# Kernel optimization log

Hardware: AMD Instinct MI355X
Metric: run time of the kernel (lower is better)

Reference implementation:

```python
import jax, jax.numpy as jnp
import numpy as np

N_NODES = 100000
N_EDGES = 1600000
D_IN = 128
D_HID = 64
D_EMB = 64
EDGE_DIM = 2 * D_EMB  # 128
N_CASES = 4
BATCH = 16384
BN_EPS = 1e-5


def gcn_conv(x, src, dst, n, W, b):
    # PyG GCNConv: linear transform, add self-loops, sym-normalized aggregation
    h = x @ W  # [N, out]
    loop = jnp.arange(n, dtype=src.dtype)
    s = jnp.concatenate([src, loop])
    d = jnp.concatenate([dst, loop])
    deg = jax.ops.segment_sum(jnp.ones(s.shape[0], dtype=h.dtype), d, num_segments=n)
    dinv = jnp.where(deg > 0, deg ** -0.5, 0.0)
    norm = dinv[s] * dinv[d]  # [E+N]
    msg = h[s] * norm[:, None]
    return jax.ops.segment_sum(msg, d, num_segments=n) + b


def batchnorm(h, gamma, beta):
    # BatchNorm1d in training mode: biased batch statistics over nodes
    mu = h.mean(0)
    var = jnp.mean((h - mu) ** 2, axis=0)
    return (h - mu) * jax.lax.rsqrt(var + BN_EPS) * gamma + beta


def gcn_net(x, src, dst, n, W1, b1, g, be, W2, b2):
    h = gcn_conv(x, src, dst, n, W1, b1)
    h = jax.nn.relu(batchnorm(h, g, be))
    return gcn_conv(h, src, dst, n, W2, b2)


def setup_inputs() -> dict:
    key = jax.random.key(0)
    ks = jax.random.split(key, 20)
    inp = {
        "x": jax.random.normal(ks[0], (N_NODES, D_IN), dtype=jnp.float32),
        "edge_index": jax.random.randint(ks[1], (2, N_EDGES), 0, N_NODES, dtype=jnp.int32),
        "users_tensor": jax.random.randint(ks[2], (BATCH,), 0, 50000, dtype=jnp.int64) if jax.config.jax_enable_x64 else jax.random.randint(ks[2], (BATCH,), 0, 50000, dtype=jnp.int32),
        "items_tensor": jax.random.randint(ks[3], (BATCH,), 0, N_NODES, dtype=jnp.int32),
    }
    s = 0.05
    # generalized GCN params
    inp["W1g"] = jax.random.normal(ks[4], (D_IN, D_HID), dtype=jnp.float32) * s
    inp["b1g"] = jnp.zeros((D_HID,), jnp.float32)
    inp["g1g"] = jnp.ones((D_HID,), jnp.float32)
    inp["be1g"] = jnp.zeros((D_HID,), jnp.float32)
    inp["W2g"] = jax.random.normal(ks[5], (D_HID, D_EMB), dtype=jnp.float32) * s
    inp["b2g"] = jnp.zeros((D_EMB,), jnp.float32)
    # specific GCN params
    inp["W1s"] = jax.random.normal(ks[6], (D_IN, D_HID), dtype=jnp.float32) * s
    inp["b1s"] = jnp.zeros((D_HID,), jnp.float32)
    inp["g1s"] = jnp.ones((D_HID,), jnp.float32)
    inp["be1s"] = jnp.zeros((D_HID,), jnp.float32)
    inp["W2s"] = jax.random.normal(ks[7], (D_HID, D_EMB), dtype=jnp.float32) * s
    inp["b2s"] = jnp.zeros((D_EMB,), jnp.float32)
    # fusion gate (note: original forward uses hidden1 for BOTH inputs)
    inp["Wf1"] = jax.random.normal(ks[8], (EDGE_DIM, EDGE_DIM), dtype=jnp.float32) * s
    inp["Wsig"] = jax.random.normal(ks[9], (2 * EDGE_DIM, 1), dtype=jnp.float32) * s
    # heads
    inp["Wtc"] = jax.random.normal(ks[10], (EDGE_DIM, N_CASES), dtype=jnp.float32) * s
    inp["btc"] = jnp.zeros((N_CASES,), jnp.float32)
    inp["Wp"] = jax.random.normal(ks[11], (EDGE_DIM, 2), dtype=jnp.float32) * s
    inp["bp"] = jnp.zeros((2,), jnp.float32)
    return inp


def reference(x, edge_index, users_tensor, items_tensor,
              W1g, b1g, g1g, be1g, W2g, b2g,
              W1s, b1s, g1s, be1s, W2s, b2s,
              Wf1, Wsig, Wtc, btc, Wp, bp):
    n = x.shape[0]
    src, dst = edge_index[0], edge_index[1]

    nodes_gen = gcn_net(x, src, dst, n, W1g, b1g, g1g, be1g, W2g, b2g)  # [N, D_EMB]
    nodes_spec = gcn_net(x, src, dst, n, W1s, b1s, g1s, be1s, W2s, b2s)

    gen = jnp.concatenate([nodes_gen[users_tensor], nodes_gen[items_tensor]], axis=1)   # [B, 2E]
    spec = jnp.concatenate([nodes_spec[users_tensor], nodes_spec[items_tensor]], axis=1)

    h1 = jnp.tanh(gen @ Wf1)
    h2 = jnp.tanh(spec @ Wf1)  # original reuses hidden1
    z = jax.nn.sigmoid(jnp.concatenate([h1, h2], axis=1) @ Wsig)  # [B,1]
    fused = z * h1 + (1.0 - z) * h2

    link_output = fused @ Wp + bp
    generalized_output = gen @ Wtc + btc
    return (link_output, generalized_output)
```

## Files before the change

### kernel.cpp

```cpp
#include <hip/hip_runtime.h>
#include <hip/hip_bf16.h>


#define ELL_CAP 64
#define BCAP 8192
#define ACHUNK 5120

typedef __attribute__((ext_vector_type(8))) short short8v;
typedef __attribute__((ext_vector_type(4))) float f32x4;

static __device__ __forceinline__ unsigned short f2bf(float f) {
  unsigned u = __float_as_uint(f);
  unsigned r = (u + 0x7fffu + ((u >> 16) & 1u)) >> 16;
  return (unsigned short)r;
}
static __device__ __forceinline__ unsigned packbf(float a, float b) {
  return (unsigned)f2bf(a) | ((unsigned)f2bf(b) << 16);
}
static __device__ __forceinline__ float bflo(unsigned u) {
  return __uint_as_float(u << 16);
}
static __device__ __forceinline__ float bfhi(unsigned u) {
  return __uint_as_float(u & 0xffff0000u);
}
static __device__ __forceinline__ float bf2f(short s) {
  return __uint_as_float((unsigned)(unsigned short)s << 16);
}

__global__ void k_prep(const float* __restrict__ x, unsigned* __restrict__ bff,
                       int* __restrict__ gbump, float* __restrict__ stats,
                       const float* __restrict__ W1g, const float* __restrict__ b1g,
                       const float* __restrict__ W1s, const float* __restrict__ b1s,
                       const float* __restrict__ W2g, const float* __restrict__ b2g,
                       const float* __restrict__ W2s, const float* __restrict__ b2s,
                       const float* __restrict__ Wf1,
                       short* __restrict__ Wb1, short* __restrict__ Wb2,
                       short* __restrict__ WbH, float* __restrict__ bc1,
                       float* __restrict__ bc2, int n, int NB) {
  int idx = blockIdx.x * 256 + threadIdx.x;
  int n16 = n * 16;
  if (idx < n16) {
    const float4* f4 = (const float4*)x;
    float4 a = f4[idx * 2], b = f4[idx * 2 + 1];
    uint4 o;
    o.x = packbf(a.x, a.y);
    o.y = packbf(a.z, a.w);
    o.z = packbf(b.x, b.y);
    o.w = packbf(b.z, b.w);
    ((uint4*)bff)[idx] = o;
  }
  if (idx < 16384) {
    int k = idx >> 7, c = idx & 127;
    int pi = (k >> 3) * 1024 + c * 8 + (k & 7);
    float w1 = (c < 64) ? W1g[k * 64 + c] : W1s[k * 64 + (c - 64)];
    Wb1[pi] = (short)f2bf(w1);
    float w2 = 0.f;
    if (k < 64 && c < 64) w2 = W2g[k * 64 + c];
    else if (k >= 64 && c >= 64) w2 = W2s[(k - 64) * 64 + (c - 64)];
    Wb2[pi] = (short)f2bf(w2);
    WbH[pi] = (short)f2bf(Wf1[k * 128 + c]);
  }
  if (idx < 128) {
    bc1[idx] = (idx < 64) ? b1g[idx] : b1s[idx - 64];
    bc2[idx] = (idx < 64) ? b2g[idx] : b2s[idx - 64];
  }
  if (idx < NB) gbump[idx] = idx * BCAP;
  if (idx < 2048) stats[idx] = 0.f;
}

__global__ __launch_bounds__(256) void k_bucketA(
    const int* __restrict__ src, const int* __restrict__ dst,
    int* __restrict__ gbump, unsigned* __restrict__ ebuf, int E, int NB) {
  __shared__ int hist[512];
  __shared__ int gbase[512];
  int t = threadIdx.x;
  int e0 = blockIdx.x * ACHUNK;
  int m = min(ACHUNK, E - e0);
  for (int b = t; b < NB; b += 256) hist[b] = 0;
  __syncthreads();
  for (int i = t; i < m; i += 256) atomicAdd(&hist[dst[e0 + i] >> 8], 1);
  __syncthreads();
  for (int b = t; b < NB; b += 256) {
    gbase[b] = hist[b] ? atomicAdd(&gbump[b], hist[b]) : 0;
    hist[b] = 0;
  }
  __syncthreads();
  for (int i = t; i < m; i += 256) {
    int d = dst[e0 + i];
    int s = src[e0 + i];
    int b = d >> 8;
    int off = gbase[b] + atomicAdd(&hist[b], 1);
    if (off < (b + 1) * BCAP)
      ebuf[off] = ((unsigned)s << 8) | (unsigned)(d & 255);
  }
}

__global__ __launch_bounds__(256) void k_csrB(
    const unsigned* __restrict__ ebuf, const int* __restrict__ gbump,
    int* __restrict__ cnt, float* __restrict__ dinv, int* __restrict__ col,
    int n) {
  __shared__ int lbump[256];
  int b = blockIdx.x;
  lbump[threadIdx.x] = 0;
  __syncthreads();
  int base = b * BCAP;
  int m = min(gbump[b] - base, BCAP);
  for (int i = threadIdx.x; i < m; i += 256) {
    unsigned p = ebuf[base + i];
    int dloc = p & 255;
    int slot = atomicAdd(&lbump[dloc], 1);
    if (slot < ELL_CAP)
      col[(b * 256 + dloc) * ELL_CAP + slot] = (int)(p >> 8);
  }
  __syncthreads();
  int node = b * 256 + threadIdx.x;
  if (node < n) {
    int c = lbump[threadIdx.x];
    cnt[node] = min(c, ELL_CAP);
    dinv[node] = rsqrtf((float)(c + 1));
  }
}

template <bool STATS, bool CBF16, bool BN>
__global__ __launch_bounds__(256) void k_aggemm(
    const unsigned* __restrict__ featb, const int* __restrict__ cnt,
    const float* __restrict__ dinv, const int* __restrict__ col,
    const short* __restrict__ Wb, const float* __restrict__ bias,
    void* __restrict__ Cvp, int n, float* __restrict__ stats,
    const float* __restrict__ g1g, const float* __restrict__ be1g,
    const float* __restrict__ g1s, const float* __restrict__ be1s,
    float inv_n) {
  __shared__ __align__(16) unsigned abuf[4096];
  __shared__ float shs[128], shq[128];
  __shared__ float sc_sh[128], sf_sh[128];
  if (STATS && threadIdx.x < 128) { shs[threadIdx.x] = 0.f; shq[threadIdx.x] = 0.f; }
  if (BN) {
    int c = threadIdx.x;
    if (c < 128) {
      float s = 0.f, q = 0.f;
#pragma unroll
      for (int k = 0; k < 8; k++) {
        s += stats[k * 256 + c];
        q += stats[k * 256 + 128 + c];
      }
      float mu = s * inv_n;
      float var = q * inv_n - mu * mu;
      float gam = (c < 64) ? g1g[c] : g1s[c - 64];
      float bet = (c < 64) ? be1g[c] : be1s[c - 64];
      float scv = gam * rsqrtf(var + 1e-5f);
      sc_sh[c] = scv;
      sf_sh[c] = bet - mu * scv;
    }
  }
  __syncthreads();

  {
    int t = threadIdx.x & 15;
    int ng = threadIdx.x >> 4;
    float sc[8], sf[8];
    if (BN) {
#pragma unroll
      for (int j = 0; j < 8; j++) {
        sc[j] = sc_sh[8 * t + j];
        sf[j] = sf_sh[8 * t + j];
      }
    }
    const uint4* f4 = (const uint4*)featb;
    uint4* ab4 = (uint4*)abuf;
    for (int sub = 0; sub < 4; sub++) {
      int r = sub * 16 + ng;
      int node = blockIdx.x * 64 + r;
      int nodec = min(node, n - 1);
      float di = dinv[nodec];
      float acc[8];
      {
        uint4 sv = f4[nodec * 16 + t];
        float f[8] = {bflo(sv.x), bfhi(sv.x), bflo(sv.y), bfhi(sv.y),
                      bflo(sv.z), bfhi(sv.z), bflo(sv.w), bfhi(sv.w)};
#pragma unroll
        for (int j = 0; j < 8; j++) {
          if (BN) f[j] = fmaxf(f[j] * sc[j] + sf[j], 0.f);
          acc[j] = f[j] * di;
        }
      }
      int m = cnt[nodec];
      const int4* cl = (const int4*)&col[nodec * ELL_CAP];
      int i = 0;
      for (; i + 4 <= m; i += 4) {
        int4 c4 = cl[i >> 2];
        int ss[4] = {c4.x, c4.y, c4.z, c4.w};
#pragma unroll
        for (int q = 0; q < 4; q++) {
          int s = ss[q];
          float w = dinv[s];
          uint4 v = f4[s * 16 + t];
          float f[8] = {bflo(v.x), bfhi(v.x), bflo(v.y), bfhi(v.y),
                        bflo(v.z), bfhi(v.z), bflo(v.w), bfhi(v.w)};
#pragma unroll
          for (int j = 0; j < 8; j++) {
            if (BN) f[j] = fmaxf(f[j] * sc[j] + sf[j], 0.f);
            acc[j] += f[j] * w;
          }
        }
      }
      for (; i < m; ++i) {
        int s = col[nodec * ELL_CAP + i];
        float w = dinv[s];
        uint4 v = f4[s * 16 + t];
        float f[8] = {bflo(v.x), bfhi(v.x), bflo(v.y), bfhi(v.y),
                      bflo(v.z), bfhi(v.z), bflo(v.w), bfhi(v.w)};
#pragma unroll
        for (int j = 0; j < 8; j++) {
          if (BN) f[j] = fmaxf(f[j] * sc[j] + sf[j], 0.f);
          acc[j] += f[j] * w;
        }
      }
      uint4 o;
      o.x = packbf(acc[0] * di, acc[1] * di);
      o.y = packbf(acc[2] * di, acc[3] * di);
      o.z = packbf(acc[4] * di, acc[5] * di);
      o.w = packbf(acc[6] * di, acc[7] * di);
      ab4[r * 16 + (t ^ (r & 7))] = o;
    }
  }
  __syncthreads();

  int lane = threadIdx.x & 63;
  int wv = threadIdx.x >> 6;
  int l15 = lane & 15;
  int l4 = lane >> 4;
  int lrow = wv * 16 + l15;
  int row = blockIdx.x * 64 + lrow;
  bool valid = row < n;
  const uint4* ab4 = (const uint4*)abuf;

  short8v afr[4];
#pragma unroll
  for (int ks = 0; ks < 4; ks++)
    afr[ks] = *(const short8v*)&ab4[lrow * 16 + ((ks * 4 + l4) ^ (lrow & 7))];

#pragma unroll 1
  for (int nt = 0; nt < 8; nt++) {
    f32x4 a = (f32x4){0.f, 0.f, 0.f, 0.f};
#pragma unroll
    for (int ks = 0; ks < 4; ks++) {
      int kb = ks * 4 + l4;
      short8v w = *(const short8v*)&Wb[kb * 1024 + (nt * 16 + l15) * 8];
      a = __builtin_amdgcn_mfma_f32_16x16x32_bf16(w, afr[ks], a, 0, 0, 0);
    }
    int c0 = nt * 16 + l4 * 4;
    float o[4];
#pragma unroll
    for (int r = 0; r < 4; r++) o[r] = a[r];
    if (bias) {
      float4 bv = *(const float4*)(bias + c0);
      o[0] += bv.x; o[1] += bv.y; o[2] += bv.z; o[3] += bv.w;
    }
    if (STATS) {
      float s[4], q[4];
#pragma unroll
      for (int r = 0; r < 4; r++) {
        s[r] = valid ? o[r] : 0.f;
        q[r] = s[r] * s[r];
      }
#pragma unroll
      for (int m = 1; m < 16; m <<= 1) {
#pragma unroll
        for (int r = 0; r < 4; r++) {
          s[r] += __shfl_xor(s[r], m, 64);
          q[r] += __shfl_xor(q[r], m, 64);
        }
      }
      if (l15 == 0) {
#pragma unroll
        for (int r = 0; r < 4; r++) {
          atomicAdd(&shs[c0 + r], s[r]);
          atomicAdd(&shq[c0 + r], q[r]);
        }
      }
    }
    if (valid) {
      if (CBF16) {
        unsigned* Cb = (unsigned*)Cvp;
        uint2 p;
        p.x = packbf(o[0], o[1]);
        p.y = packbf(o[2], o[3]);
        *(uint2*)&Cb[(size_t)row * 64 + (c0 >> 1)] = p;
      } else {
        float* Cf = (float*)Cvp;
        *(float4*)&Cf[(size_t)row * 128 + c0] = make_float4(o[0], o[1], o[2], o[3]);
      }
    }
  }
  if (STATS) {
    __syncthreads();
    if (threadIdx.x < 128) {
      float* st = stats + (blockIdx.x & 7) * 256;
      atomicAdd(&st[threadIdx.x], shs[threadIdx.x]);
      atomicAdd(&st[128 + threadIdx.x], shq[threadIdx.x]);
    }
  }
}

__global__ __launch_bounds__(256) void k_fhead(
    const unsigned short* __restrict__ nodesb,
    const int* __restrict__ users, const int* __restrict__ items,
    const short* __restrict__ WbH, const float* __restrict__ Wsig,
    const float* __restrict__ Wtc, const float* __restrict__ btc,
    const float* __restrict__ Wp, const float* __restrict__ bp,
    float* __restrict__ out, int B) {
  __shared__ short Wl[16384];
  __shared__ float WsigL[256], WpL[256], WtcL[512];
  {
    const uint4* s4 = (const uint4*)WbH;
    uint4* d4 = (uint4*)Wl;
    for (int i = threadIdx.x; i < 2048; i += 256) d4[i] = s4[i];
    if (threadIdx.x < 256) {
      WsigL[threadIdx.x] = Wsig[threadIdx.x];
      WpL[threadIdx.x] = Wp[threadIdx.x];
    }
    for (int i = threadIdx.x; i < 512; i += 256) WtcL[i] = Wtc[i];
  }
  __syncthreads();
  int lane = threadIdx.x & 63;
  int wv = threadIdx.x >> 6;
  int l15 = lane & 15;
  int l4 = lane >> 4;
  int row = blockIdx.x * 64 + wv * 16 + l15;
  int rc = min(row, B - 1);
  int u = users[rc], it = items[rc];
  const short* pu = (const short*)nodesb + u * 128;
  const short* pi = (const short*)nodesb + it * 128;

  short8v ag[4], as[4];
#pragma unroll
  for (int ks = 0; ks < 4; ks++) {
    int k = ks * 32 + l4 * 8;
    const short* pg = (ks < 2) ? (pu + k) : (pi + (k - 64));
    const short* ps = (ks < 2) ? (pu + 64 + k) : (pi + k);
    ag[ks] = *(const short8v*)pg;
    as[ks] = *(const short8v*)ps;
  }

  f32x4 a1[8], a2[8];
#pragma unroll
  for (int nt = 0; nt < 8; nt++) {
    a1[nt] = (f32x4){0.f, 0.f, 0.f, 0.f};
    a2[nt] = (f32x4){0.f, 0.f, 0.f, 0.f};
  }
#pragma unroll
  for (int nt = 0; nt < 8; nt++) {
#pragma unroll
    for (int ks = 0; ks < 4; ks++) {
      int kb = ks * 4 + l4;
      short8v w = *(const short8v*)&Wl[kb * 1024 + (nt * 16 + l15) * 8];
      a1[nt] = __builtin_amdgcn_mfma_f32_16x16x32_bf16(w, ag[ks], a1[nt], 0, 0, 0);
      a2[nt] = __builtin_amdgcn_mfma_f32_16x16x32_bf16(w, as[ks], a2[nt], 0, 0, 0);
    }
  }

  float zp = 0.f;
#pragma unroll
  for (int nt = 0; nt < 8; nt++) {
    int c0 = nt * 16 + l4 * 4;
#pragma unroll
    for (int r = 0; r < 4; r++) {
      float h1 = tanhf(a1[nt][r]);
      float h2 = tanhf(a2[nt][r]);
      a1[nt][r] = h1;
      a2[nt][r] = h2;
      zp += h1 * WsigL[c0 + r] + h2 * WsigL[128 + c0 + r];
    }
  }
  zp += __shfl_xor(zp, 16, 64);
  zp += __shfl_xor(zp, 32, 64);
  float z = 1.f / (1.f + expf(-zp));

  float p0 = 0.f, p1 = 0.f;
#pragma unroll
  for (int nt = 0; nt < 8; nt++) {
    int c0 = nt * 16 + l4 * 4;
#pragma unroll
    for (int r = 0; r < 4; r++) {
      float fu = z * a1[nt][r] + (1.f - z) * a2[nt][r];
      p0 += fu * WpL[(c0 + r) * 2];
      p1 += fu * WpL[(c0 + r) * 2 + 1];
    }
  }
  float t0 = 0.f, t1 = 0.f, t2 = 0.f, t3 = 0.f;
#pragma unroll
  for (int ks = 0; ks < 4; ks++) {
    int kbase = ks * 32 + l4 * 8;
#pragma unroll
    for (int j = 0; j < 8; j++) {
      float gv = bf2f(ag[ks][j]);
      int c = kbase + j;
      t0 += gv * WtcL[c * 4];
      t1 += gv * WtcL[c * 4 + 1];
      t2 += gv * WtcL[c * 4 + 2];
      t3 += gv * WtcL[c * 4 + 3];
    }
  }
  p0 += __shfl_xor(p0, 16, 64); p0 += __shfl_xor(p0, 32, 64);
  p1 += __shfl_xor(p1, 16, 64); p1 += __shfl_xor(p1, 32, 64);
  t0 += __shfl_xor(t0, 16, 64); t0 += __shfl_xor(t0, 32, 64);
  t1 += __shfl_xor(t1, 16, 64); t1 += __shfl_xor(t1, 32, 64);
  t2 += __shfl_xor(t2, 16, 64); t2 += __shfl_xor(t2, 32, 64);
  t3 += __shfl_xor(t3, 16, 64); t3 += __shfl_xor(t3, 32, 64);

  if (l4 == 0 && row < B) {
    out[row * 2] = p0 + bp[0];
    out[row * 2 + 1] = p1 + bp[1];
    float* go = out + 2 * B;
    go[row * 4] = t0 + btc[0];
    go[row * 4 + 1] = t1 + btc[1];
    go[row * 4 + 2] = t2 + btc[2];
    go[row * 4 + 3] = t3 + btc[3];
  }
}

extern "C" void kernel_launch(void* const* d_in, const int* in_sizes, int n_in,
                              void* d_out, int out_size, void* d_ws, size_t ws_size,
                              hipStream_t stream) {
  const float* x = (const float*)d_in[0];
  const int* ei = (const int*)d_in[1];
  const int* users = (const int*)d_in[2];
  const int* items = (const int*)d_in[3];
  const float* W1g = (const float*)d_in[4];
  const float* b1g = (const float*)d_in[5];
  const float* g1g = (const float*)d_in[6];
  const float* be1g = (const float*)d_in[7];
  const float* W2g = (const float*)d_in[8];
  const float* b2g = (const float*)d_in[9];
  const float* W1s = (const float*)d_in[10];
  const float* b1s = (const float*)d_in[11];
  const float* g1s = (const float*)d_in[12];
  const float* be1s = (const float*)d_in[13];
  const float* W2s = (const float*)d_in[14];
  const float* b2s = (const float*)d_in[15];
  const float* Wf1 = (const float*)d_in[16];
  const float* Wsig = (const float*)d_in[17];
  const float* Wtc = (const float*)d_in[18];
  const float* btc = (const float*)d_in[19];
  const float* Wp = (const float*)d_in[20];
  const float* bp = (const float*)d_in[21];

  int n = in_sizes[0] / 128;
  int E = in_sizes[1] / 2;
  int B = in_sizes[2];
  int NB = (n + 255) >> 8;
  const int* srcp = ei;
  const int* dstp = ei + E;
  float* out = (float*)d_out;

  char* w = (char*)d_ws;
  auto alloc = [&](size_t bytes) -> char* {
    char* p = w;
    w += (bytes + 255) & ~(size_t)255;
    return p;
  };
  unsigned* bff = (unsigned*)alloc((size_t)n * 128 * 2);
  float* big1 = (float*)alloc((size_t)n * 128 * 4);
  int* col = (int*)alloc((size_t)n * ELL_CAP * 4);
  unsigned* ebuf = (unsigned*)alloc((size_t)NB * BCAP * 4);
  int* cnt = (int*)alloc((size_t)n * 4);
  float* dinv = (float*)alloc((size_t)n * 4);
  int* gbump = (int*)alloc(512 * 4);
  short* Wb1 = (short*)alloc(16384 * 2);
  short* Wb2 = (short*)alloc(16384 * 2);
  short* WbH = (short*)alloc(16384 * 2);
  float* bc1 = (float*)alloc(512);
  float* bc2 = (float*)alloc(512);
  float* stats = (float*)alloc(2048 * 4);

  k_prep<<<(n * 16 + 255) / 256, 256, 0, stream>>>(
      x, bff, gbump, stats, W1g, b1g, W1s, b1s, W2g, b2g, W2s, b2s, Wf1,
      Wb1, Wb2, WbH, bc1, bc2, n, NB);
  k_bucketA<<<(E + ACHUNK - 1) / ACHUNK, 256, 0, stream>>>(srcp, dstp, gbump, ebuf, E, NB);
  k_csrB<<<NB, 256, 0, stream>>>(ebuf, gbump, cnt, dinv, col, n);

  unsigned* hb = (unsigned*)big1;
  unsigned short* nodesb = (unsigned short*)bff;

  k_aggemm<true, true, false><<<(n + 63) / 64, 256, 0, stream>>>(
      bff, cnt, dinv, col, Wb1, bc1, hb, n, stats,
      nullptr, nullptr, nullptr, nullptr, 0.f);

  k_aggemm<false, true, true><<<(n + 63) / 64, 256, 0, stream>>>(
      hb, cnt, dinv, col, Wb2, bc2, nodesb, n, stats,
      g1g, be1g, g1s, be1s, 1.f / (float)n);

  k_fhead<<<(B + 63) / 64, 256, 0, stream>>>(nodesb, users, items, WbH, Wsig,
                                             Wtc, btc, Wp, bp, out, B);
}
```

Measured before the change: 242.2 us.

## Overlap x-to-bf16 conversion with edge bucketing; drop block barrier in aggregation

The fp32-to-bf16 conversion of x moves out of the prep kernel and into extra blocks of the edge-bucketing kernel, so the two independent memory-bound jobs share one launch and the prep kernel shrinks to 64 blocks. In the aggregation+GEMM kernel, each wave now gathers exactly the 16 rows it later feeds to MFMA. This lets the __syncthreads between the gather and the GEMM become a per-wave lgkmcnt wait plus a sched_barrier. The barrier removal depends on the row mapping lining up exactly with each wave's MFMA rows in LDS.

```diff
diff --git a/kernel.cpp b/kernel.cpp
--- a/kernel.cpp
+++ b/kernel.cpp
@@ -27,8 +27,7 @@
   return __uint_as_float((unsigned)(unsigned short)s << 16);
 }
 
-__global__ void k_prep(const float* __restrict__ x, unsigned* __restrict__ bff,
-                       int* __restrict__ gbump, float* __restrict__ stats,
+__global__ void k_prep(int* __restrict__ gbump, float* __restrict__ stats,
                        const float* __restrict__ W1g, const float* __restrict__ b1g,
                        const float* __restrict__ W1s, const float* __restrict__ b1s,
                        const float* __restrict__ W2g, const float* __restrict__ b2g,
@@ -36,19 +35,8 @@
                        const float* __restrict__ Wf1,
                        short* __restrict__ Wb1, short* __restrict__ Wb2,
                        short* __restrict__ WbH, float* __restrict__ bc1,
-                       float* __restrict__ bc2, int n, int NB) {
+                       float* __restrict__ bc2, int NB) {
   int idx = blockIdx.x * 256 + threadIdx.x;
-  int n16 = n * 16;
-  if (idx < n16) {
-    const float4* f4 = (const float4*)x;
-    float4 a = f4[idx * 2], b = f4[idx * 2 + 1];
-    uint4 o;
-    o.x = packbf(a.x, a.y);
-    o.y = packbf(a.z, a.w);
-    o.z = packbf(b.x, b.y);
-    o.w = packbf(b.z, b.w);
-    ((uint4*)bff)[idx] = o;
-  }
   if (idx < 16384) {
     int k = idx >> 7, c = idx & 127;
     int pi = (k >> 3) * 1024 + c * 8 + (k & 7);
@@ -68,9 +56,25 @@
   if (idx < 2048) stats[idx] = 0.f;
 }
 
-__global__ __launch_bounds__(256) void k_bucketA(
+__global__ __launch_bounds__(256) void k_bucketAX(
     const int* __restrict__ src, const int* __restrict__ dst,
-    int* __restrict__ gbump, unsigned* __restrict__ ebuf, int E, int NB) {
+    int* __restrict__ gbump, unsigned* __restrict__ ebuf, int E, int NB,
+    const float* __restrict__ x, unsigned* __restrict__ bff, int n16,
+    int nblkA) {
+  if ((int)blockIdx.x >= nblkA) {
+    int i = ((int)blockIdx.x - nblkA) * 256 + threadIdx.x;
+    if (i < n16) {
+      const float4* f4 = (const float4*)x;
+      float4 a = f4[i * 2], b = f4[i * 2 + 1];
+      uint4 o;
+      o.x = packbf(a.x, a.y);
+      o.y = packbf(a.z, a.w);
+      o.z = packbf(b.x, b.y);
+      o.w = packbf(b.z, b.w);
+      ((uint4*)bff)[i] = o;
+    }
+    return;
+  }
   __shared__ int hist[512];
   __shared__ int gbase[512];
   int t = threadIdx.x;
@@ -154,9 +158,12 @@
   }
   __syncthreads();
 
+  int lane = threadIdx.x & 63;
+  int wv = threadIdx.x >> 6;
+  int t = lane & 15;
+  int g = (lane >> 4) & 3;
+
   {
-    int t = threadIdx.x & 15;
-    int ng = threadIdx.x >> 4;
     float sc[8], sf[8];
     if (BN) {
 #pragma unroll
@@ -167,8 +174,8 @@
     }
     const uint4* f4 = (const uint4*)featb;
     uint4* ab4 = (uint4*)abuf;
-    for (int sub = 0; sub < 4; sub++) {
-      int r = sub * 16 + ng;
+    for (int it = 0; it < 4; ++it) {
+      int r = wv * 16 + it * 4 + g;
       int node = blockIdx.x * 64 + r;
       int nodec = min(node, n - 1);
       float di = dinv[nodec];
@@ -223,10 +230,9 @@
       ab4[r * 16 + (t ^ (r & 7))] = o;
     }
   }
-  __syncthreads();
-
-  int lane = threadIdx.x & 63;
-  int wv = threadIdx.x >> 6;
+  asm volatile("s_waitcnt lgkmcnt(0)" ::: "memory");
+  __builtin_amdgcn_sched_barrier(0);
+
   int l15 = lane & 15;
   int l4 = lane >> 4;
   int lrow = wv * 16 + l15;
@@ -473,10 +479,13 @@
   float* bc2 = (float*)alloc(512);
   float* stats = (float*)alloc(2048 * 4);
 
-  k_prep<<<(n * 16 + 255) / 256, 256, 0, stream>>>(
-      x, bff, gbump, stats, W1g, b1g, W1s, b1s, W2g, b2g, W2s, b2s, Wf1,
-      Wb1, Wb2, WbH, bc1, bc2, n, NB);
-  k_bucketA<<<(E + ACHUNK - 1) / ACHUNK, 256, 0, stream>>>(srcp, dstp, gbump, ebuf, E, NB);
+  int nblkA = (E + ACHUNK - 1) / ACHUNK;
+  int nblkX = (n * 16 + 255) / 256;
+
+  k_prep<<<64, 256, 0, stream>>>(gbump, stats, W1g, b1g, W1s, b1s, W2g, b2g,
+                                 W2s, b2s, Wf1, Wb1, Wb2, WbH, bc1, bc2, NB);
+  k_bucketAX<<<nblkA + nblkX, 256, 0, stream>>>(srcp, dstp, gbump, ebuf, E, NB,
+                                                x, bff, n * 16, nblkA);
   k_csrB<<<NB, 256, 0, stream>>>(ebuf, gbump, cnt, dinv, col, n);
 
   unsigned* hb = (unsigned*)big1;
```

Result: slower. 252.7 us (+4.3%).
